# Optimization experiments

Measured on AMD Instinct MI355X. Metric: run time of the kernel, lower is better.

Reference implementation:

```python
import jax, jax.numpy as jnp
import numpy as np

H = 16        # num heads
NOPE = 128    # qk_nope_head_dim
ROPE = 64     # qk_rope_head_dim
VD = 128      # v_head_dim
HID = 2048    # hidden_dim
QLR = 1536    # q_lora_rank
KVLR = 512    # kv_lora_rank
B = 4
S = 1024
EPS = 1e-6


def setup_inputs() -> dict:
    key = jax.random.key(0)
    ks = jax.random.split(key, 8)
    def w(k, o, i):
        return jax.random.normal(k, (o, i), jnp.float32) * 0.02
    x = jax.random.normal(ks[0], (B * S, HID), jnp.float32)
    wq_a = w(ks[1], QLR, HID)
    w_qa_ln = jnp.ones((QLR,), jnp.float32)
    wq_b = w(ks[2], H * (NOPE + ROPE), QLR)
    wkv_a = w(ks[3], KVLR + ROPE, HID)
    w_kva_ln = jnp.ones((KVLR,), jnp.float32)
    wk_b = w(ks[4], H * NOPE, KVLR)
    wv_b = w(ks[5], H * VD, KVLR)
    wo = w(ks[6], HID, H * VD)
    # interleaved RoPE tables: [S, ROPE//2]
    pos = jnp.arange(S, dtype=jnp.float32)
    inv_freq = 1.0 / (10000.0 ** (jnp.arange(0, ROPE, 2, dtype=jnp.float32) / ROPE))
    freqs = pos[:, None] * inv_freq[None, :]
    rotary_sin = jnp.sin(freqs)
    rotary_cos = jnp.cos(freqs)
    seqstarts = jnp.arange(B + 1, dtype=jnp.int32) * S
    return dict(x=x, wq_a=wq_a, w_qa_ln=w_qa_ln, wq_b=wq_b, wkv_a=wkv_a,
                w_kva_ln=w_kva_ln, wk_b=wk_b, wv_b=wv_b, wo=wo,
                rotary_sin=rotary_sin, rotary_cos=rotary_cos, seqstarts=seqstarts)


def rmsnorm(h, w):
    return h * jax.lax.rsqrt(jnp.mean(h * h, axis=-1, keepdims=True) + EPS) * w


def rope_interleaved(t, sin, cos):
    # t: [B,S,h,ROPE]; sin/cos: [S,ROPE//2]; rotate adjacent pairs (even, odd)
    tr = t.reshape(t.shape[:-1] + (ROPE // 2, 2))
    e, o = tr[..., 0], tr[..., 1]
    s = sin[None, :, None, :]
    c = cos[None, :, None, :]
    return jnp.stack([e * c - o * s, e * s + o * c], axis=-1).reshape(t.shape)


def reference(x, wq_a, w_qa_ln, wq_b, wkv_a, w_kva_ln, wk_b, wv_b, wo,
              rotary_sin, rotary_cos, seqstarts):
    b = seqstarts.shape[0] - 1
    s = x.shape[0] // b
    # low-rank Q: hidden -> q_lora -> H*(nope+rope)
    q = rmsnorm(x @ wq_a.T, w_qa_ln) @ wq_b.T
    q = q.reshape(b, s, H, NOPE + ROPE)
    q_nope, q_pe = q[..., :NOPE], q[..., NOPE:]
    # low-rank KV: hidden -> kv_lora + rope (k_pe shared across heads)
    kv = x @ wkv_a.T
    ckv = rmsnorm(kv[:, :KVLR], w_kva_ln)
    k_pe = kv[:, KVLR:].reshape(b, s, 1, ROPE)
    k_nope = (ckv @ wk_b.T).reshape(b, s, H, NOPE)
    v = (ckv @ wv_b.T).reshape(b, s, H, VD)
    q_pe = rope_interleaved(q_pe, rotary_sin, rotary_cos)
    k_pe = rope_interleaved(k_pe, rotary_sin, rotary_cos)
    scale = 1.0 / np.sqrt(NOPE + ROPE).astype(np.float32)
    scores = (jnp.einsum('bqhd,bkhd->bhqk', q_nope, k_nope)
              + jnp.einsum('bqhd,bkjd->bhqk', q_pe, k_pe)) * scale
    causal = jnp.tril(jnp.ones((s, s), bool))
    scores = jnp.where(causal[None, None], scores, jnp.float32(-1e30))
    p = jax.nn.softmax(scores, axis=-1)
    out = jnp.einsum('bhqk,bkhd->bqhd', p, v).reshape(b * s, H * VD)
    return out @ wo.T
```

## Files before the change

kernel.cpp:

```cpp
#include <hip/hip_runtime.h>
#include <stdint.h>

typedef __bf16 bf16;
typedef __bf16 bf16x8 __attribute__((ext_vector_type(8)));
typedef float floatx4 __attribute__((ext_vector_type(4)));
typedef float floatx16 __attribute__((ext_vector_type(16)));

#define HH     16
#define DNOPE  128
#define DROPE  64
#define DV     128
#define DQK    192
#define HID    2048
#define QLR    1536
#define KVLR   512
#define BB     4
#define SS     1024
#define NTOK   4096
#define XOUTW  2176
#define EPSF   1e-6f

__device__ inline void cvt_store4(bf16* dst, float a, float b, float c, float d) {
  union { bf16 h[4]; uint2 u; } t;
  t.h[0] = (bf16)a; t.h[1] = (bf16)b; t.h[2] = (bf16)c; t.h[3] = (bf16)d;
  *(uint2*)dst = t.u;
}

__device__ inline void gl_lds16(const bf16* g, bf16* l) {
  __builtin_amdgcn_global_load_lds(
      (const __attribute__((address_space(1))) void*)g,
      (__attribute__((address_space(3))) void*)l, 16, 0, 0);
}

__global__ __launch_bounds__(256) void cvt_all(
    const float* __restrict__ x, const float* __restrict__ wq_a,
    const float* __restrict__ wkv_a, const float* __restrict__ wq_b,
    const float* __restrict__ wk_b, const float* __restrict__ wv_b,
    const float* __restrict__ wo, bf16* __restrict__ xb,
    bf16* __restrict__ wA, bf16* __restrict__ wqbb,
    bf16* __restrict__ wkvB, bf16* __restrict__ wob, float scaleq) {
  const int blk = blockIdx.x, tid = threadIdx.x;
  const float* s; bf16* d; int rel; float sc = 1.0f;
  if (blk < 8192)       { rel = blk;         s = x;    d = xb; }
  else if (blk < 11264) { rel = blk - 8192;  s = wq_a; d = wA; }
  else if (blk < 12544) {
    rel = blk - 11264;
    int i = (rel * 256 + tid) << 2;
    bf16* dd = wA + 3145728;
    if ((i >> 11) < 576) {
      float4 v = *(const float4*)(wkv_a + i);
      cvt_store4(dd + i, v.x, v.y, v.z, v.w);
    } else {
      *(uint2*)(dd + i) = make_uint2(0u, 0u);
    }
    return;
  }
  else if (blk < 17152) { rel = blk - 12544; s = wq_b; d = wqbb; sc = scaleq; }
  else if (blk < 18176) { rel = blk - 17152; s = wk_b; d = wkvB; }
  else if (blk < 19200) { rel = blk - 18176; s = wv_b; d = wkvB + 1048576; }
  else                  { rel = blk - 19200; s = wo;   d = wob; }
  int i = (rel * 256 + tid) << 2;
  float4 v = *(const float4*)(s + i);
  cvt_store4(d + i, v.x * sc, v.y * sc, v.z * sc, v.w * sc);
}

template <typename TC, int EPI>
__global__ __launch_bounds__(256) void gemm_bt_bf16(
    const bf16* __restrict__ A, const bf16* __restrict__ Bw,
    TC* __restrict__ C0, bf16* __restrict__ C1, int M, int N, int K) {
  __shared__ __align__(16) bf16 As[3][128 * 32];
  __shared__ __align__(16) bf16 Bs[3][128 * 32];
  const int tid  = threadIdx.x;
  const int wave = tid >> 6, lane = tid & 63;
  const int gx = gridDim.x;
  const int fid = blockIdx.y * gx + blockIdx.x;
  const int cpx = (gx * gridDim.y) >> 3;
  const int sid = (fid & 7) * cpx + (fid >> 3);
  const int m0 = (sid % gx) << 7, n0 = (sid / gx) << 7;
  const int quad = lane >> 4, l16 = lane & 15;
  const int wm = (wave >> 1) << 6, wn = (wave & 1) << 6;

  const int srow0 = tid >> 2, g = tid & 3;
  const int gsw = g ^ ((srow0 >> 1) & 3);
  const int d0 = srow0 * 32 + (g << 3);
  const int d1 = d0 + 64 * 32;
  const bf16* gA0 = A  + (size_t)(m0 + srow0) * K + (gsw << 3);
  const bf16* gA1 = A  + (size_t)(m0 + srow0 + 64) * K + (gsw << 3);
  const bf16* gB0 = Bw + (size_t)(n0 + srow0) * K + (gsw << 3);
  const bf16* gB1 = Bw + (size_t)(n0 + srow0 + 64) * K + (gsw << 3);

  floatx4 acc[4][4];
#pragma unroll
  for (int i = 0; i < 4; i++)
#pragma unroll
    for (int j = 0; j < 4; j++) acc[i][j] = floatx4{0.f, 0.f, 0.f, 0.f};

  const int nk = K >> 5;
  gl_lds16(gA0, As[0] + d0); gl_lds16(gA1, As[0] + d1);
  gl_lds16(gB0, Bs[0] + d0); gl_lds16(gB1, Bs[0] + d1);
  gl_lds16(gA0 + 32, As[1] + d0); gl_lds16(gA1 + 32, As[1] + d1);
  gl_lds16(gB0 + 32, Bs[1] + d0); gl_lds16(gB1 + 32, Bs[1] + d1);

  const int swr = (l16 >> 1) & 3;
  int cur = 0, nx2 = 2;
  for (int kt = 0; kt < nk; kt++) {
    if (kt + 1 < nk)
      asm volatile("s_waitcnt vmcnt(4)\n\ts_barrier" ::: "memory");
    else
      asm volatile("s_waitcnt vmcnt(0)\n\ts_barrier" ::: "memory");
    if (kt + 2 < nk) {
      const size_t kk = (size_t)(kt + 2) << 5;
      gl_lds16(gA0 + kk, As[nx2] + d0); gl_lds16(gA1 + kk, As[nx2] + d1);
      gl_lds16(gB0 + kk, Bs[nx2] + d0); gl_lds16(gB1 + kk, Bs[nx2] + d1);
    }
    __builtin_amdgcn_sched_barrier(0);

    const bf16* cA = As[cur];
    const bf16* cB = Bs[cur];
    bf16x8 af[4], bv[4];
#pragma unroll
    for (int i = 0; i < 4; i++) {
      const int r = wm + (i << 4) + l16;
      af[i] = *(const bf16x8*)&cA[r * 32 + (((quad ^ swr) & 3) << 3)];
    }
#pragma unroll
    for (int j = 0; j < 4; j++) {
      const int r = wn + (j << 4) + l16;
      bv[j] = *(const bf16x8*)&cB[r * 32 + (((quad ^ swr) & 3) << 3)];
    }
#pragma unroll
    for (int i = 0; i < 4; i++)
#pragma unroll
      for (int j = 0; j < 4; j++)
        acc[i][j] = __builtin_amdgcn_mfma_f32_16x16x32_bf16(af[i], bv[j], acc[i][j], 0, 0, 0);

    cur = (cur == 2) ? 0 : cur + 1;
    nx2 = (nx2 == 2) ? 0 : nx2 + 1;
  }

  if constexpr (EPI == 1) {
    if (n0 >= 2048) {
#pragma unroll
      for (int i = 0; i < 4; i++) {
        int gm = m0 + wm + (i << 4) + (quad << 2);
        int bb = gm >> 10, s = gm & 1023;
#pragma unroll
        for (int j = 0; j < 4; j++) {
          int gn = n0 + wn + (j << 4) + l16 - 2048;
          int hh = gn >> 7, vd = gn & 127;
          union { bf16 h4[4]; uint2 u; } pk;
#pragma unroll
          for (int r = 0; r < 4; r++) pk.h4[r] = (bf16)acc[i][j][r];
          *(uint2*)(C1 + ((((size_t)bb * HH + hh) * DV + vd) << 10) + s) = pk.u;
        }
      }
      return;
    }
  }
  const int ldc = (EPI == 1) ? 2048 : N;
#pragma unroll
  for (int i = 0; i < 4; i++)
#pragma unroll
    for (int j = 0; j < 4; j++) {
      int gn = n0 + wn + (j << 4) + l16;
#pragma unroll
      for (int r = 0; r < 4; r++) {
        int gm = m0 + wm + (i << 4) + (quad << 2) + r;
        C0[(size_t)gm * ldc + gn] = (TC)acc[i][j][r];
      }
    }
}

__global__ __launch_bounds__(256) void norm_rope(
    const bf16* __restrict__ xout, const float* __restrict__ w_qa_ln,
    const float* __restrict__ w_kva_ln, bf16* __restrict__ qln,
    bf16* __restrict__ ckv, bf16* __restrict__ kpe,
    const float* __restrict__ rsin, const float* __restrict__ rcos) {
  const int blk = blockIdx.x, tid = threadIdx.x;
  if (blk < 8192) {
    const int row = blk & 4095;
    const bool isq = blk < 4096;
    const bf16* p = xout + (size_t)row * XOUTW + (isq ? 0 : QLR);
    const float* w = isq ? w_qa_ln : w_kva_ln;
    bf16* o = isq ? (qln + (size_t)row * QLR) : (ckv + (size_t)row * KVLR);
    const int L = isq ? QLR : KVLR;
    float ss = 0.f;
    for (int c = tid << 2; c < L; c += 1024) {
      union { uint2 u; bf16 h[4]; } t;
      t.u = *(const uint2*)(p + c);
#pragma unroll
      for (int r = 0; r < 4; r++) { float v = (float)t.h[r]; ss += v * v; }
    }
#pragma unroll
    for (int off = 32; off > 0; off >>= 1) ss += __shfl_down(ss, off);
    __shared__ float red[4];
    if ((tid & 63) == 0) red[tid >> 6] = ss;
    __syncthreads();
    float rs = rsqrtf((red[0] + red[1] + red[2] + red[3]) / (float)L + EPSF);
    for (int c = tid << 2; c < L; c += 1024) {
      union { uint2 u; bf16 h[4]; } t, ot;
      t.u = *(const uint2*)(p + c);
#pragma unroll
      for (int r = 0; r < 4; r++) ot.h[r] = (bf16)((float)t.h[r] * rs * w[c + r]);
      *(uint2*)(o + c) = ot.u;
    }
  } else {
    int idx = (blk - 8192) * 256 + tid;
    int i = idx & 31, row = idx >> 5;
    int pos = row & (SS - 1);
    union { uint u; bf16 h2[2]; } t;
    t.u = *(const uint*)(xout + (size_t)row * XOUTW + QLR + KVLR + (i << 1));
    float e = (float)t.h2[0], o = (float)t.h2[1];
    float c = rcos[(pos << 5) + i], s = rsin[(pos << 5) + i];
    t.h2[0] = (bf16)(e * c - o * s);
    t.h2[1] = (bf16)(e * s + o * c);
    *(uint*)(kpe + (size_t)row * DROPE + (i << 1)) = t.u;
  }
}

__global__ void rope_q(bf16* __restrict__ q, const float* __restrict__ sin_t,
                       const float* __restrict__ cos_t) {
  int idx = blockIdx.x * 256 + threadIdx.x;
  int i = idx & 31, h = (idx >> 5) & 15, row = idx >> 9;
  int pos = row & (SS - 1);
  bf16* base = q + ((size_t)row * HH + h) * DQK + DNOPE + (i << 1);
  union { uint u; bf16 h2[2]; } t;
  t.u = *(uint*)base;
  float e = (float)t.h2[0], o = (float)t.h2[1];
  float c = cos_t[(pos << 5) + i], s = sin_t[(pos << 5) + i];
  t.h2[0] = (bf16)(e * c - o * s);
  t.h2[1] = (bf16)(e * s + o * c);
  *(uint*)base = t.u;
}

__global__ __launch_bounds__(512, 2) void attn_kernel(
    const bf16* __restrict__ q, const bf16* __restrict__ knope,
    const bf16* __restrict__ kpe, const bf16* __restrict__ vT,
    bf16* __restrict__ out) {
  const int qt = 3 - blockIdx.x;
  const int q0 = qt << 8;
  const int nkt = (qt + 1) << 2;
  const int h = blockIdx.y, b = blockIdx.z;
  __shared__ __align__(16) bf16 smem[40960];
  const int tid = threadIdx.x, wave = tid >> 6, lane = tid & 63;
  const int l32 = lane & 31, hi = lane >> 5;
  const int hi4 = hi << 2;
  const int Q0w = q0 + (wave << 5);
  const int qg = Q0w + l32;

  const bf16 *gkn0, *gkn1, *gkp, *gvt0, *gvt1;
  {
    int c = wave << 1;
    int r = (c << 2) + (lane >> 4);
    int bi = (lane & 15) ^ (r & 15);
    gkn0 = knope + ((size_t)((b << 10) + r) * HH + h) * DNOPE + (bi << 3);
    r = ((c + 1) << 2) + (lane >> 4);
    bi = (lane & 15) ^ (r & 15);
    gkn1 = knope + ((size_t)((b << 10) + r) * HH + h) * DNOPE + (bi << 3);
    r = (wave << 3) + (lane >> 3);
    bi = (lane & 7) ^ (r & 7);
    gkp = kpe + (size_t)((b << 10) + r) * DROPE + (bi << 3);
    int dv = (wave << 4) + (lane >> 3);
    bi = (lane & 7) ^ (dv & 7);
    gvt0 = vT + ((((size_t)b * HH + h) * DV + dv) << 10) + (bi << 3);
    dv += 8;
    bi = (lane & 7) ^ (dv & 7);
    gvt1 = vT + ((((size_t)b * HH + h) * DV + dv) << 10) + (bi << 3);
  }
  const size_t knstep = (size_t)64 * HH * DNOPE;
  const size_t kpstep = (size_t)64 * DROPE;
  const int woff = wave << 10, woff2 = wave << 9;

  gl_lds16(gkn0, smem + woff);
  gl_lds16(gkn1, smem + woff + 512);
  gl_lds16(gkp,  smem + 8192 + woff2);
  gl_lds16(gvt0, smem + 12288 + woff);
  gl_lds16(gvt1, smem + 12288 + woff + 512);
  gkn0 += knstep; gkn1 += knstep; gkp += kpstep; gvt0 += 64; gvt1 += 64;

  bf16x8 qb[12];
  {
    const bf16* qbase =
        q + ((size_t)((b << 10) + Q0w + l32) * HH + h) * DQK + (hi << 3);
#pragma unroll
    for (int dc = 0; dc < 12; dc++)
      qb[dc] = *(const bf16x8*)(qbase + (dc << 4));
  }

  floatx16 acc[4];
#pragma unroll
  for (int g = 0; g < 4; g++)
#pragma unroll
    for (int r = 0; r < 16; r++) acc[g][r] = 0.f;
  float m_i = -1e30f, l_i = 0.f;

  for (int s = 0; s < nkt; s++) {
    const int k0 = s << 6;
    asm volatile("s_waitcnt vmcnt(0)\n\ts_barrier" ::: "memory");
    if (s + 1 < nkt) {
      bf16* bufp = smem + ((s + 1) & 1) * 20480;
      gl_lds16(gkn0, bufp + woff);
      gl_lds16(gkn1, bufp + woff + 512);
      gl_lds16(gkp,  bufp + 8192 + woff2);
      gl_lds16(gvt0, bufp + 12288 + woff);
      gl_lds16(gvt1, bufp + 12288 + woff + 512);
      gkn0 += knstep; gkn1 += knstep; gkp += kpstep; gvt0 += 64; gvt1 += 64;
    }
    __builtin_amdgcn_sched_barrier(0);
    if (k0 > Q0w + 31) continue;

    const bf16* Kn = smem + (s & 1) * 20480;
    const bf16* Kp = Kn + 8192;
    const bf16* Vt = Kn + 12288;

    floatx16 s0, s1;
#pragma unroll
    for (int r = 0; r < 16; r++) { s0[r] = 0.f; s1[r] = 0.f; }
    __builtin_amdgcn_s_setprio(1);
#pragma unroll
    for (int dc = 0; dc < 12; dc++) {
      bf16x8 ak0, ak1;
      if (dc < 8) {
        int gi = (((dc << 1) + hi) ^ (l32 & 15)) << 3;
        ak0 = *(const bf16x8*)&Kn[(l32 << 7) + gi];
        ak1 = *(const bf16x8*)&Kn[((32 + l32) << 7) + gi];
      } else {
        int gi = ((((dc - 8) << 1) + hi) ^ (l32 & 7)) << 3;
        ak0 = *(const bf16x8*)&Kp[(l32 << 6) + gi];
        ak1 = *(const bf16x8*)&Kp[((32 + l32) << 6) + gi];
      }
      s0 = __builtin_amdgcn_mfma_f32_32x32x16_bf16(ak0, qb[dc], s0, 0, 0, 0);
      s1 = __builtin_amdgcn_mfma_f32_32x32x16_bf16(ak1, qb[dc], s1, 0, 0, 0);
    }
    __builtin_amdgcn_s_setprio(0);

    if (k0 + 63 > Q0w) {
#pragma unroll
      for (int r = 0; r < 16; r++) {
        int rp = (r & 3) + ((r >> 2) << 3) + hi4;
        if (k0 + rp > qg)      s0[r] = -1e30f;
        if (k0 + 32 + rp > qg) s1[r] = -1e30f;
      }
    }

    float mx = -1e30f;
#pragma unroll
    for (int r = 0; r < 16; r++) mx = fmaxf(mx, fmaxf(s0[r], s1[r]));
    mx = fmaxf(mx, __shfl_xor(mx, 32));
    if (!__all(mx - m_i <= 8.0f)) {
      float mnew = fmaxf(m_i, mx);
      float alpha = exp2f(m_i - mnew);
      l_i *= alpha;
#pragma unroll
      for (int g = 0; g < 4; g++)
#pragma unroll
        for (int r = 0; r < 16; r++) acc[g][r] *= alpha;
      m_i = mnew;
    }
    float sum = 0.f;
#pragma unroll
    for (int r = 0; r < 16; r++) {
      float p0 = exp2f(s0[r] - m_i), p1 = exp2f(s1[r] - m_i);
      s0[r] = p0; s1[r] = p1;
      sum += p0 + p1;
    }
    sum += __shfl_xor(sum, 32);
    l_i += sum;

    uint P32[2][4][2];
#pragma unroll
    for (int hh = 0; hh < 4; hh++) {
      union { bf16 e[2]; uint u; } w0, w1, w2, w3;
      w0.e[0] = (bf16)s0[(hh << 2) + 0]; w0.e[1] = (bf16)s0[(hh << 2) + 1];
      w1.e[0] = (bf16)s0[(hh << 2) + 2]; w1.e[1] = (bf16)s0[(hh << 2) + 3];
      w2.e[0] = (bf16)s1[(hh << 2) + 0]; w2.e[1] = (bf16)s1[(hh << 2) + 1];
      w3.e[0] = (bf16)s1[(hh << 2) + 2]; w3.e[1] = (bf16)s1[(hh << 2) + 3];
      P32[0][hh][0] = w0.u; P32[0][hh][1] = w1.u;
      P32[1][hh][0] = w2.u; P32[1][hh][1] = w3.u;
    }
    bf16x8 bp[4];
#pragma unroll
    for (int c = 0; c < 4; c++) {
      const int t = c >> 1, sb = c & 1;
      uint send0 = hi ? P32[t][(sb << 1)][0] : P32[t][(sb << 1) + 1][0];
      uint send1 = hi ? P32[t][(sb << 1)][1] : P32[t][(sb << 1) + 1][1];
      uint r0 = __shfl_xor(send0, 32);
      uint r1 = __shfl_xor(send1, 32);
      union { uint u[4]; bf16x8 v; } f;
      if (hi == 0) {
        f.u[0] = P32[t][(sb << 1)][0]; f.u[1] = P32[t][(sb << 1)][1];
        f.u[2] = r0;                   f.u[3] = r1;
      } else {
        f.u[0] = r0;                         f.u[1] = r1;
        f.u[2] = P32[t][(sb << 1) + 1][0];   f.u[3] = P32[t][(sb << 1) + 1][1];
      }
      bp[c] = f.v;
    }

    __builtin_amdgcn_s_setprio(1);
#pragma unroll
    for (int c = 0; c < 4; c++) {
      const int gsw = (((c << 1) + hi) ^ (l32 & 7)) << 3;
#pragma unroll
      for (int g = 0; g < 4; g++) {
        bf16x8 av = *(const bf16x8*)&Vt[(((g << 5) + l32) << 6) + gsw];
        acc[g] = __builtin_amdgcn_mfma_f32_32x32x16_bf16(av, bp[c], acc[g], 0, 0, 0);
      }
    }
    __builtin_amdgcn_s_setprio(0);
  }

  const float invl = 1.0f / l_i;
  const int tok = (b << 10) + Q0w + l32;
  bf16* obase = out + ((size_t)tok * HH + h) * DV + hi4;
#pragma unroll
  for (int g = 0; g < 4; g++)
#pragma unroll
    for (int t = 0; t < 4; t++) {
      union { bf16 h4[4]; uint2 u; } pk;
#pragma unroll
      for (int r = 0; r < 4; r++)
        pk.h4[r] = (bf16)(acc[g][(t << 2) + r] * invl);
      *(uint2*)(obase + (g << 5) + (t << 3)) = pk.u;
    }
}

extern "C" void kernel_launch(void* const* d_in, const int* in_sizes, int n_in,
                              void* d_out, int out_size, void* d_ws, size_t ws_size,
                              hipStream_t stream) {
  (void)in_sizes; (void)n_in; (void)out_size; (void)ws_size;
  const float* x        = (const float*)d_in[0];
  const float* wq_a     = (const float*)d_in[1];
  const float* w_qa_ln  = (const float*)d_in[2];
  const float* wq_b     = (const float*)d_in[3];
  const float* wkv_a    = (const float*)d_in[4];
  const float* w_kva_ln = (const float*)d_in[5];
  const float* wk_b     = (const float*)d_in[6];
  const float* wv_b     = (const float*)d_in[7];
  const float* wo       = (const float*)d_in[8];
  const float* rsin     = (const float*)d_in[9];
  const float* rcos     = (const float*)d_in[10];
  float* out = (float*)d_out;

  char* ws = (char*)d_ws;
  bf16* xb    = (bf16*)(ws + 0);
  bf16* attnb = (bf16*)(ws + 0);
  bf16* xout  = (bf16*)(ws + 16777216);
  bf16* knope = (bf16*)(ws + 16777216);
  bf16* q     = (bf16*)(ws + 34603008);
  bf16* qln   = (bf16*)(ws + 59768832);
  bf16* vT    = (bf16*)(ws + 59768832);
  bf16* wA    = (bf16*)(ws + 76546048);
  bf16* wqbb  = (bf16*)(ws + 85458944);
  bf16* wkvB  = (bf16*)(ws + 94896128);
  bf16* wob   = (bf16*)(ws + 99090432);
  bf16* ckv   = (bf16*)(ws + 107479040);
  bf16* kpe   = (bf16*)(ws + 111673344);

  const float SCALEQ = (1.0f / sqrtf(192.0f)) * 1.44269504088896f;

  dim3 blk(256);
  cvt_all<<<23296, blk, 0, stream>>>(x, wq_a, wkv_a, wq_b, wk_b, wv_b, wo,
                                     xb, wA, wqbb, wkvB, wob, SCALEQ);
  gemm_bt_bf16<bf16, 0><<<dim3(32, 17), blk, 0, stream>>>(
      xb, wA, xout, nullptr, NTOK, XOUTW, HID);
  norm_rope<<<8704, blk, 0, stream>>>(xout, w_qa_ln, w_kva_ln, qln, ckv, kpe,
                                      rsin, rcos);
  gemm_bt_bf16<bf16, 0><<<dim3(32, 24), blk, 0, stream>>>(
      qln, wqbb, q, nullptr, NTOK, HH * DQK, QLR);
  rope_q<<<8192, blk, 0, stream>>>(q, rsin, rcos);
  gemm_bt_bf16<bf16, 1><<<dim3(32, 32), blk, 0, stream>>>(
      ckv, wkvB, knope, vT, NTOK, 4096, KVLR);
  attn_kernel<<<dim3(4, HH, BB), dim3(512), 0, stream>>>(
      q, knope, kpe, vT, attnb);
  gemm_bt_bf16<float, 0><<<dim3(32, 16), blk, 0, stream>>>(
      attnb, wob, out, nullptr, NTOK, HID, HID);
}
```

Before: 404.3 us.

## Add 256x256-tile 512-thread GEMM kernel for q_b, kv_b and output projections

Adds a new GEMM kernel that computes a 256x256 output tile per block with 8 waves, triple-buffered LDS prefetch and MFMA priority raising through s_setprio. It replaces the 128x128 GEMM for three of the four projection GEMMs. The larger tiles raise arithmetic intensity and cut global and LDS traffic per FLOP. In exchange each block uses more LDS and registers, and grids shrink to 128–256 blocks, which may leave CUs underused on the 256-CU MI355X.

```diff
diff --git a/kernel.cpp b/kernel.cpp
--- a/kernel.cpp
+++ b/kernel.cpp
@@ -138,10 +138,101 @@
     nx2 = (nx2 == 2) ? 0 : nx2 + 1;
   }
 
+  const int ldc = (EPI == 1) ? 2048 : N;
+#pragma unroll
+  for (int i = 0; i < 4; i++)
+#pragma unroll
+    for (int j = 0; j < 4; j++) {
+      int gn = n0 + wn + (j << 4) + l16;
+#pragma unroll
+      for (int r = 0; r < 4; r++) {
+        int gm = m0 + wm + (i << 4) + (quad << 2) + r;
+        C0[(size_t)gm * ldc + gn] = (TC)acc[i][j][r];
+      }
+    }
+}
+
+template <typename TC, int EPI>
+__global__ __launch_bounds__(512) void gemm256_bt(
+    const bf16* __restrict__ A, const bf16* __restrict__ Bw,
+    TC* __restrict__ C0, bf16* __restrict__ C1, int M, int N, int K) {
+  __shared__ __align__(16) bf16 As[3][256 * 32];
+  __shared__ __align__(16) bf16 Bs[3][256 * 32];
+  const int tid  = threadIdx.x;
+  const int wave = tid >> 6, lane = tid & 63;
+  const int quad = lane >> 4, l16 = lane & 15;
+  const int gx = gridDim.x;
+  const int fid = blockIdx.y * gx + blockIdx.x;
+  const int cpx = (gx * gridDim.y) >> 3;
+  const int sid = (fid & 7) * cpx + (fid >> 3);
+  const int m0 = (sid % gx) << 8, n0 = (sid / gx) << 8;
+  const int wm = (wave >> 2) << 7;
+  const int wn = (wave & 3) << 6;
+
+  const int srow = tid >> 2, g = tid & 3;
+  const int gsw = g ^ ((srow >> 1) & 3);
+  const int d0 = srow * 32 + (g << 3);
+  const int d1 = d0 + 128 * 32;
+  const bf16* gA0 = A  + (size_t)(m0 + srow) * K + (gsw << 3);
+  const bf16* gA1 = gA0 + (size_t)128 * K;
+  const bf16* gB0 = Bw + (size_t)(n0 + srow) * K + (gsw << 3);
+  const bf16* gB1 = gB0 + (size_t)128 * K;
+
+  floatx4 acc[8][4];
+#pragma unroll
+  for (int i = 0; i < 8; i++)
+#pragma unroll
+    for (int j = 0; j < 4; j++) acc[i][j] = floatx4{0.f, 0.f, 0.f, 0.f};
+
+  const int nk = K >> 5;
+  gl_lds16(gA0, As[0] + d0); gl_lds16(gA1, As[0] + d1);
+  gl_lds16(gB0, Bs[0] + d0); gl_lds16(gB1, Bs[0] + d1);
+  gl_lds16(gA0 + 32, As[1] + d0); gl_lds16(gA1 + 32, As[1] + d1);
+  gl_lds16(gB0 + 32, Bs[1] + d0); gl_lds16(gB1 + 32, Bs[1] + d1);
+
+  const int swr = (l16 >> 1) & 3;
+  int cur = 0, nx2 = 2;
+  for (int kt = 0; kt < nk; kt++) {
+    if (kt + 1 < nk)
+      asm volatile("s_waitcnt vmcnt(4)\n\ts_barrier" ::: "memory");
+    else
+      asm volatile("s_waitcnt vmcnt(0)\n\ts_barrier" ::: "memory");
+    if (kt + 2 < nk) {
+      const size_t kk = (size_t)(kt + 2) << 5;
+      gl_lds16(gA0 + kk, As[nx2] + d0); gl_lds16(gA1 + kk, As[nx2] + d1);
+      gl_lds16(gB0 + kk, Bs[nx2] + d0); gl_lds16(gB1 + kk, Bs[nx2] + d1);
+    }
+    __builtin_amdgcn_sched_barrier(0);
+
+    const bf16* cA = As[cur];
+    const bf16* cB = Bs[cur];
+    bf16x8 af[8], bv[4];
+#pragma unroll
+    for (int i = 0; i < 8; i++) {
+      const int r = wm + (i << 4) + l16;
+      af[i] = *(const bf16x8*)&cA[r * 32 + (((quad ^ swr) & 3) << 3)];
+    }
+#pragma unroll
+    for (int j = 0; j < 4; j++) {
+      const int r = wn + (j << 4) + l16;
+      bv[j] = *(const bf16x8*)&cB[r * 32 + (((quad ^ swr) & 3) << 3)];
+    }
+    __builtin_amdgcn_s_setprio(1);
+#pragma unroll
+    for (int i = 0; i < 8; i++)
+#pragma unroll
+      for (int j = 0; j < 4; j++)
+        acc[i][j] = __builtin_amdgcn_mfma_f32_16x16x32_bf16(af[i], bv[j], acc[i][j], 0, 0, 0);
+    __builtin_amdgcn_s_setprio(0);
+
+    cur = (cur == 2) ? 0 : cur + 1;
+    nx2 = (nx2 == 2) ? 0 : nx2 + 1;
+  }
+
   if constexpr (EPI == 1) {
     if (n0 >= 2048) {
 #pragma unroll
-      for (int i = 0; i < 4; i++) {
+      for (int i = 0; i < 8; i++) {
         int gm = m0 + wm + (i << 4) + (quad << 2);
         int bb = gm >> 10, s = gm & 1023;
 #pragma unroll
@@ -159,7 +250,7 @@
   }
   const int ldc = (EPI == 1) ? 2048 : N;
 #pragma unroll
-  for (int i = 0; i < 4; i++)
+  for (int i = 0; i < 8; i++)
 #pragma unroll
     for (int j = 0; j < 4; j++) {
       int gn = n0 + wn + (j << 4) + l16;
@@ -466,13 +557,13 @@
       xb, wA, xout, nullptr, NTOK, XOUTW, HID);
   norm_rope<<<8704, blk, 0, stream>>>(xout, w_qa_ln, w_kva_ln, qln, ckv, kpe,
                                       rsin, rcos);
-  gemm_bt_bf16<bf16, 0><<<dim3(32, 24), blk, 0, stream>>>(
+  gemm256_bt<bf16, 0><<<dim3(16, 12), dim3(512), 0, stream>>>(
       qln, wqbb, q, nullptr, NTOK, HH * DQK, QLR);
   rope_q<<<8192, blk, 0, stream>>>(q, rsin, rcos);
-  gemm_bt_bf16<bf16, 1><<<dim3(32, 32), blk, 0, stream>>>(
+  gemm256_bt<bf16, 1><<<dim3(16, 16), dim3(512), 0, stream>>>(
       ckv, wkvB, knope, vT, NTOK, 4096, KVLR);
   attn_kernel<<<dim3(4, HH, BB), dim3(512), 0, stream>>>(
       q, knope, kpe, vT, attnb);
-  gemm_bt_bf16<float, 0><<<dim3(32, 16), blk, 0, stream>>>(
+  gemm256_bt<float, 0><<<dim3(16, 8), dim3(512), 0, stream>>>(
       attnb, wob, out, nullptr, NTOK, HID, HID);
 }
```

After: 445.9 us. 10.3% more time.
